# Performance work log

Hardware: AMD Instinct MI355X
Metric: run time of the kernel (lower is better)

The kernel has to match this reference:

```python
import jax, jax.numpy as jnp
import numpy as np

N_NODES = 100000
N_EDGES = 400000
D = 128

def _mlp_ln(x, W1, b1, W2, b2, W3, b3, gamma, beta):
    h = jax.nn.relu(x @ W1 + b1)
    h = jax.nn.relu(h @ W2 + b2)
    h = h @ W3 + b3
    mu = jnp.mean(h, axis=-1, keepdims=True)
    var = jnp.var(h, axis=-1, keepdims=True)
    return (h - mu) * jax.lax.rsqrt(var + 1e-5) * gamma + beta


def setup_inputs() -> dict:
    key = jax.random.key(0)
    ks = jax.random.split(key, 12)
    s = lambda fan_in: 1.0 / np.sqrt(fan_in)
    inp = {
        'node_features': jax.random.normal(ks[0], (1, N_NODES, D), jnp.float32),
        'edge_features': jax.random.normal(ks[1], (1, N_EDGES, D), jnp.float32),
        'senders': jax.random.randint(ks[2], (1, N_EDGES), 0, N_NODES, jnp.int32),
        'receivers': jax.random.randint(ks[3], (1, N_EDGES), 0, N_NODES, jnp.int32),
        'e_W1': jax.random.normal(ks[4], (3 * D, D), jnp.float32) * s(3 * D),
        'e_b1': jnp.zeros((D,), jnp.float32),
        'e_W2': jax.random.normal(ks[5], (D, D), jnp.float32) * s(D),
        'e_b2': jnp.zeros((D,), jnp.float32),
        'e_W3': jax.random.normal(ks[6], (D, D), jnp.float32) * s(D),
        'e_b3': jnp.zeros((D,), jnp.float32),
        'e_gamma': jnp.ones((D,), jnp.float32),
        'e_beta': jnp.zeros((D,), jnp.float32),
        'n_W1': jax.random.normal(ks[7], (2 * D, D), jnp.float32) * s(2 * D),
        'n_b1': jnp.zeros((D,), jnp.float32),
        'n_W2': jax.random.normal(ks[8], (D, D), jnp.float32) * s(D),
        'n_b2': jnp.zeros((D,), jnp.float32),
        'n_W3': jax.random.normal(ks[9], (D, D), jnp.float32) * s(D),
        'n_b3': jnp.zeros((D,), jnp.float32),
        'n_gamma': jnp.ones((D,), jnp.float32),
        'n_beta': jnp.zeros((D,), jnp.float32),
    }
    return inp


def reference(node_features, edge_features, senders, receivers,
              e_W1, e_b1, e_W2, e_b2, e_W3, e_b3, e_gamma, e_beta,
              n_W1, n_b1, n_W2, n_b2, n_W3, n_b3, n_gamma, n_beta):
    # batch dim is 1; indexing matches torch.index_select(dim=1, senders[0])
    snd = senders[0]
    rcv = receivers[0]
    nodes = node_features[0]          # [N, D]
    edges = edge_features[0]          # [E, D]

    # edge update: gather, concat, edge MLP
    edge_in = jnp.concatenate([nodes[snd], nodes[rcv], edges], axis=-1)  # [E, 3D]
    new_edges = _mlp_ln(edge_in, e_W1, e_b1, e_W2, e_b2, e_W3, e_b3, e_gamma, e_beta)

    # node update: segment-sum aggregate to receivers, concat, node MLP
    agg = jax.ops.segment_sum(new_edges, rcv, num_segments=nodes.shape[0])  # [N, D]
    node_in = jnp.concatenate([nodes, agg], axis=-1)                        # [N, 2D]
    new_nodes = _mlp_ln(node_in, n_W1, n_b1, n_W2, n_b2, n_W3, n_b3, n_gamma, n_beta)

    # residuals
    new_nodes = new_nodes + nodes
    new_edges = new_edges + edges
    return new_nodes[None], new_edges[None]
```

## Files before the change

### kernel.cpp

```cpp
#include <hip/hip_runtime.h>
#include <stdint.h>

#define NN 100000
#define NE 400000
#define SCAN_B 391

typedef __attribute__((ext_vector_type(4))) float f32x4;
typedef __attribute__((ext_vector_type(8))) short bf16x8;

__device__ __forceinline__ short f2b(float x){
  union { float f; uint32_t u; } v; v.f = x;
  uint32_t r = v.u + 0x7FFFu + ((v.u >> 16) & 1u);
  return (short)(r >> 16);
}
__device__ __forceinline__ float b2f(short x){
  union { uint32_t u; float f; } v; v.u = ((uint32_t)(unsigned short)x) << 16; return v.f;
}
__device__ __forceinline__ bf16x8 pack_bf8(f32x4 a, f32x4 b){
  bf16x8 r;
  r[0]=f2b(a[0]); r[1]=f2b(a[1]); r[2]=f2b(a[2]); r[3]=f2b(a[3]);
  r[4]=f2b(b[0]); r[5]=f2b(b[1]); r[6]=f2b(b[2]); r[7]=f2b(b[3]);
  return r;
}

__global__ void pack_all(const float* __restrict__ eW1, const float* __restrict__ eW2,
                         const float* __restrict__ eW3, const float* __restrict__ nW1,
                         const float* __restrict__ nW2, const float* __restrict__ nW3,
                         short* __restrict__ dst){
  int o = blockIdx.x*256 + threadIdx.x;
  int seg = o >> 14, rem = o & 16383;
  int kt = rem >> 12, g = (rem >> 10) & 3, n = (rem >> 3) & 127, j = rem & 7;
  int k = kt*32 + g*8 + j;
  const float* src = eW1; int koff = 0;
  switch(seg){
    case 0: src=eW1; koff=0;   break;
    case 1: src=eW1; koff=128; break;
    case 2: src=eW1; koff=256; break;
    case 3: src=eW2; break;
    case 4: src=eW3; break;
    case 5: src=nW1; koff=0;   break;
    case 6: src=nW1; koff=128; break;
    case 7: src=nW2; break;
    case 8: src=nW3; break;
  }
  dst[o] = f2b(src[(size_t)(koff+k)*128 + n]);
}

__global__ void k_count(const int* __restrict__ rcv, int* __restrict__ counts){
  int e = blockIdx.x*256 + threadIdx.x;
  if (e < NE) atomicAdd(&counts[rcv[e]], 1);
}
__global__ void k_psum(const int* __restrict__ counts, int* __restrict__ psums){
  __shared__ int red[256];
  int t = threadIdx.x, i = blockIdx.x*256 + t;
  red[t] = (i < NN) ? counts[i] : 0;
  __syncthreads();
  for (int d=128; d; d>>=1){ if (t<d) red[t] += red[t+d]; __syncthreads(); }
  if (!t) psums[blockIdx.x] = red[0];
}
__global__ __launch_bounds__(512) void k_scanp(const int* __restrict__ psums, int* __restrict__ bbase){
  __shared__ int ps[512];
  int t = threadIdx.x;
  int v = (t < SCAN_B) ? psums[t] : 0;
  ps[t] = v; __syncthreads();
  for (int d=1; d<512; d<<=1){
    int x = (t>=d) ? ps[t-d] : 0;
    __syncthreads();
    ps[t] += x;
    __syncthreads();
  }
  if (t < SCAN_B) bbase[t] = ps[t] - v;
}
__global__ void k_local(const int* __restrict__ counts, const int* __restrict__ bbase,
                        int* __restrict__ offsets, int* __restrict__ cursor){
  __shared__ int ps[256];
  int t = threadIdx.x, i = blockIdx.x*256 + t;
  int v = (i < NN) ? counts[i] : 0;
  ps[t] = v; __syncthreads();
  for (int d=1; d<256; d<<=1){
    int x = (t>=d) ? ps[t-d] : 0;
    __syncthreads();
    ps[t] += x;
    __syncthreads();
  }
  int excl = bbase[blockIdx.x] + ps[t] - v;
  if (i < NN){ offsets[i] = excl; cursor[i] = excl; }
  if (i == 0) offsets[NN] = NE;
}
__global__ void k_scatter(const int* __restrict__ rcv, int* __restrict__ cursor,
                          int* __restrict__ pos){
  int e = blockIdx.x*256 + threadIdx.x;
  if (e < NE) pos[e] = atomicAdd(&cursor[rcv[e]], 1);
}

__global__ __launch_bounds__(512,4) void compute_T(
    const float* __restrict__ nodef, const short* __restrict__ wp,
    short* __restrict__ Tt, int nrows)
{
  __shared__ __align__(16) short Ws[16384];
  const int tid=threadIdx.x, lane=tid&63, wid=tid>>6, l16=lane&15, hi=lane>>4;
  const int row0 = blockIdx.x*128;
  const int arow_l = wid*16 + l16;
  const int arow_c = min(row0 + arow_l, nrows-1);
  const float* s = nodef + (size_t)arow_c*128;

  bf16x8 af[4];
  #pragma unroll
  for (int kt=0; kt<4; kt++){
    int ko = kt*32 + hi*8;
    af[kt] = pack_bf8(*(const f32x4*)(s+ko), *(const f32x4*)(s+ko+4));
  }
  int4 w[4];
  #pragma unroll
  for (int i=0;i<4;i++) w[i] = ((const int4*)wp)[tid + 512*i];

  for (int o=0; o<2; o++){
    if (o) __syncthreads();
    #pragma unroll
    for (int i=0;i<4;i++) ((int4*)Ws)[tid + 512*i] = w[i];
    if (o < 1){
      #pragma unroll
      for (int i=0;i<4;i++) w[i] = ((const int4*)(wp + 16384))[tid + 512*i];
    }
    __syncthreads();
    f32x4 acc[8];
    #pragma unroll
    for (int t=0;t<8;t++) acc[t] = (f32x4)(0.0f);
    #pragma unroll
    for (int kt=0;kt<4;kt++){
      #pragma unroll
      for (int t=0;t<8;t++){
        bf16x8 bw = *(const bf16x8*)&Ws[kt*4096 + hi*1024 + (t*16+l16)*8];
        acc[t] = __builtin_amdgcn_mfma_f32_16x16x32_bf16(af[kt], bw, acc[t], 0,0,0);
      }
    }
    __syncthreads();
    #pragma unroll
    for (int t=0;t<8;t++){
      int col = t*16 + l16;
      #pragma unroll
      for (int r=0;r<4;r++){
        int row = wid*16 + hi*4 + r;
        *(short*)((char*)Ws + row*256 + ((col*2) ^ ((row&7)<<4))) = f2b(acc[t][r]);
      }
    }
    #pragma unroll
    for (int u=0;u<4;u++){
      int q = lane + u*64;
      int r16 = q >> 4, c = q & 15;
      int rl = wid*16 + r16;
      int grow = row0 + rl;
      if (grow < nrows){
        bf16x8 v = *(const bf16x8*)((char*)Ws + rl*256 + ((c*16) ^ ((rl&7)<<4)));
        *(bf16x8*)(Tt + (size_t)grow*256 + o*128 + c*8) = v;
      }
    }
  }
}

#define WSTAGE(NEXT) do{ __syncthreads(); \
  _Pragma("unroll") for(int i=0;i<4;i++) ((int4*)Ws)[tid + 512*i] = w[i]; \
  if ((NEXT) != nullptr){ _Pragma("unroll") for(int i=0;i<4;i++) w[i] = ((const int4*)(NEXT))[tid + 512*i]; } \
  __syncthreads(); }while(0)

#define MM_G() do{ _Pragma("unroll") for(int kt=0;kt<4;kt++){ \
  _Pragma("unroll") for(int t=0;t<8;t++){ \
    bf16x8 bw = *(const bf16x8*)&Ws[kt*4096 + hi*1024 + (t*16+l16)*8]; \
    acc[t] = __builtin_amdgcn_mfma_f32_16x16x32_bf16(afg[kt], bw, acc[t], 0,0,0);} } }while(0)

#define MM_H() do{ _Pragma("unroll") for(int kt=0;kt<4;kt++){ \
  bf16x8 afv = *(const bf16x8*)((char*)HGs + arow_l*256 + ((kt*64 + hi*16) ^ ((arow_l&7)<<4))); \
  _Pragma("unroll") for(int t=0;t<8;t++){ \
    bf16x8 bw = *(const bf16x8*)&Ws[kt*4096 + hi*1024 + (t*16+l16)*8]; \
    acc[t] = __builtin_amdgcn_mfma_f32_16x16x32_bf16(afv, bw, acc[t], 0,0,0);} } }while(0)

#define EPI_RELU(BP, ADDG) do{ \
  _Pragma("unroll") for (int t=0;t<8;t++){ \
    int col=t*16+l16; float bb=(BP)[col]; \
    _Pragma("unroll") for (int r=0;r<4;r++){ \
      int row=wid*16+hi*4+r; \
      float g=0.0f; \
      if (ADDG) g=b2f(*(const short*)((char*)HGs+row*256+((col*2)^((row&7)<<4)))); \
      float v=fmaxf(acc[t][r]+g+bb,0.0f); \
      *(short*)((char*)HGs+row*256+((col*2)^((row&7)<<4)))=f2b(v); \
      acc[t][r]=0.0f; \
    } } }while(0)

template<int MODE>
__global__ __launch_bounds__(512,4) void gnb_mlp(
    const float* __restrict__ nodef, const float* __restrict__ edgef,
    const int* __restrict__ snd, const int* __restrict__ rcv,
    const int* __restrict__ off, const int* __restrict__ pos,
    const short* __restrict__ Tt, short* __restrict__ Ey,
    const short* __restrict__ W1a, const short* __restrict__ W1b,
    const short* __restrict__ W2, const short* __restrict__ W3,
    const float* __restrict__ b1p, const float* __restrict__ b2p, const float* __restrict__ b3p,
    const float* __restrict__ gmp, const float* __restrict__ btp,
    float* __restrict__ outp, int nrows)
{
  __shared__ __align__(16) short Ws[16384];
  __shared__ __align__(16) short HGs[16384];

  const int tid=threadIdx.x, lane=tid&63, wid=tid>>6, l16=lane&15, hi=lane>>4;
  const int row0 = blockIdx.x*128;
  const int arow_l = wid*16 + l16;
  const int arow_c = min(row0 + arow_l, nrows-1);

  int4 w[4];
  #pragma unroll
  for (int i=0;i<4;i++) w[i] = ((const int4*)W1a)[tid + 512*i];

  if (MODE==0){
    bf16x8 ga[4], gb[4];
    #pragma unroll
    for (int u=0;u<4;u++){
      int q = tid + u*512, gr = q >> 4, c = q & 15;
      int grow = row0 + gr;
      int si = snd[grow], ri = rcv[grow];
      ga[u] = *(const bf16x8*)(Tt + (size_t)si*256 + c*8);
      gb[u] = *(const bf16x8*)(Tt + (size_t)ri*256 + 128 + c*8);
    }
    #pragma unroll
    for (int u=0;u<4;u++){
      int q = tid + u*512, gr = q >> 4, c = q & 15;
      bf16x8 o8;
      #pragma unroll
      for (int j=0;j<8;j++) o8[j] = f2b(b2f(ga[u][j]) + b2f(gb[u][j]));
      *(bf16x8*)((char*)HGs + gr*256 + ((c*16) ^ ((gr&7)<<4))) = o8;
    }
  } else {
    #pragma unroll
    for (int u=0;u<4;u++){
      int q = tid + u*512, gr = q >> 4, c = q & 15;
      int grow = row0 + gr;
      float s8[8] = {0,0,0,0,0,0,0,0};
      if (grow < nrows){
        int jb = off[grow], je = off[grow+1];
        for (int j=jb;j<je;j++){
          bf16x8 v = *(const bf16x8*)(Ey + (size_t)j*128 + c*8);
          #pragma unroll
          for (int k=0;k<8;k++) s8[k] += b2f(v[k]);
        }
      }
      bf16x8 o8;
      #pragma unroll
      for (int k=0;k<8;k++) o8[k] = f2b(s8[k]);
      *(bf16x8*)((char*)HGs + gr*256 + ((c*16) ^ ((gr&7)<<4))) = o8;
    }
  }

  WSTAGE((MODE==0) ? W2 : W1b);

  const float* s1 = (MODE==0) ? (edgef + (size_t)arow_c*128) : (nodef + (size_t)arow_c*128);
  bf16x8 afg[4];
  #pragma unroll
  for (int kt=0;kt<4;kt++){
    int ko = kt*32 + hi*8;
    afg[kt] = pack_bf8(*(const f32x4*)(s1+ko), *(const f32x4*)(s1+ko+4));
  }

  f32x4 acc[8];
  #pragma unroll
  for (int t=0;t<8;t++) acc[t] = (f32x4)(0.0f);

  MM_G();
  if (MODE==1){
    WSTAGE(W2);
    MM_H();
  }
  EPI_RELU(b1p, (MODE==0));
  WSTAGE(W3);
  MM_H();
  EPI_RELU(b2p, false);
  WSTAGE((const short*)nullptr);
  MM_H();

  float ps[4] = {0,0,0,0}, pq[4] = {0,0,0,0};
  #pragma unroll
  for (int t=0;t<8;t++){
    float bb = b3p[t*16+l16];
    #pragma unroll
    for (int r=0;r<4;r++){
      float v = acc[t][r] + bb;
      acc[t][r] = v;
      ps[r] += v; pq[r] += v*v;
    }
  }
  #pragma unroll
  for (int m=1;m<16;m<<=1){
    #pragma unroll
    for (int r=0;r<4;r++){
      ps[r] += __shfl_xor(ps[r], m);
      pq[r] += __shfl_xor(pq[r], m);
    }
  }
  float mu[4], rs[4];
  #pragma unroll
  for (int r=0;r<4;r++){
    mu[r] = ps[r] * (1.0f/128.0f);
    float var = pq[r] * (1.0f/128.0f) - mu[r]*mu[r];
    rs[r] = rsqrtf(var + 1e-5f);
  }

  #pragma unroll
  for (int t=0;t<8;t++){
    int col = t*16 + l16;
    float gm = gmp[col], be = btp[col];
    #pragma unroll
    for (int r=0;r<4;r++){
      float y = (acc[t][r]-mu[r])*rs[r]*gm + be;
      int row = wid*16 + hi*4 + r;
      *(short*)((char*)HGs + row*256 + ((col*2) ^ ((row&7)<<4))) = f2b(y);
    }
  }

  #pragma unroll
  for (int u=0;u<4;u++){
    int q = lane + u*64;
    int r16 = q >> 4, c = q & 15;
    int rl = wid*16 + r16;
    int grow = row0 + rl;
    bf16x8 v = *(const bf16x8*)((char*)HGs + rl*256 + ((c*16) ^ ((rl&7)<<4)));
    if (MODE==0){
      const float* ef = edgef + (size_t)grow*128 + c*8;
      f32x4 e0 = *(const f32x4*)ef, e1 = *(const f32x4*)(ef+4);
      f32x4 o0, o1;
      #pragma unroll
      for (int j=0;j<4;j++){ o0[j] = b2f(v[j]) + e0[j]; o1[j] = b2f(v[j+4]) + e1[j]; }
      float* op = outp + (size_t)grow*128 + c*8;
      *(f32x4*)op = o0; *(f32x4*)(op+4) = o1;
      int p = pos[grow];
      *(bf16x8*)(Ey + (size_t)p*128 + c*8) = v;
    } else {
      if (grow < nrows){
        const float* nf = nodef + (size_t)grow*128 + c*8;
        f32x4 e0 = *(const f32x4*)nf, e1 = *(const f32x4*)(nf+4);
        f32x4 o0, o1;
        #pragma unroll
        for (int j=0;j<4;j++){ o0[j] = b2f(v[j]) + e0[j]; o1[j] = b2f(v[j+4]) + e1[j]; }
        float* op = outp + (size_t)grow*128 + c*8;
        *(f32x4*)op = o0; *(f32x4*)(op+4) = o1;
      }
    }
  }
}

extern "C" void kernel_launch(void* const* d_in, const int* in_sizes, int n_in,
                              void* d_out, int out_size, void* d_ws, size_t ws_size,
                              hipStream_t stream)
{
  (void)in_sizes; (void)n_in; (void)out_size; (void)ws_size;
  const float* nodef = (const float*)d_in[0];
  const float* edgef = (const float*)d_in[1];
  const int*   snd   = (const int*)d_in[2];
  const int*   rcv   = (const int*)d_in[3];
  const float* eW1 = (const float*)d_in[4];
  const float* eb1 = (const float*)d_in[5];
  const float* eW2 = (const float*)d_in[6];
  const float* eb2 = (const float*)d_in[7];
  const float* eW3 = (const float*)d_in[8];
  const float* eb3 = (const float*)d_in[9];
  const float* egm = (const float*)d_in[10];
  const float* ebt = (const float*)d_in[11];
  const float* nW1 = (const float*)d_in[12];
  const float* nb1 = (const float*)d_in[13];
  const float* nW2 = (const float*)d_in[14];
  const float* nb2 = (const float*)d_in[15];
  const float* nW3 = (const float*)d_in[16];
  const float* nb3 = (const float*)d_in[17];
  const float* ngm = (const float*)d_in[18];
  const float* nbt = (const float*)d_in[19];

  char* wsb = (char*)d_ws;
  short* Tt = (short*)wsb;
  short* Ey = (short*)(wsb + (size_t)NN*256*2);
  int* counts  = (int*)(wsb + (size_t)NN*256*2 + (size_t)NE*128*2);
  int* offsets = counts + NN;
  int* cursor  = offsets + NN + 8;
  int* psums   = cursor + NN;
  int* bbase   = psums + 512;
  int* pos     = bbase + 512;
  short* wp    = (short*)(pos + NE);

  hipMemsetAsync(counts, 0, (size_t)NN*4, stream);
  k_count<<<(NE+255)/256,256,0,stream>>>(rcv, counts);
  k_psum<<<SCAN_B,256,0,stream>>>(counts, psums);
  k_scanp<<<1,512,0,stream>>>(psums, bbase);
  k_local<<<SCAN_B,256,0,stream>>>(counts, bbase, offsets, cursor);
  k_scatter<<<(NE+255)/256,256,0,stream>>>(rcv, cursor, pos);

  pack_all<<<576,256,0,stream>>>(eW1,eW2,eW3,nW1,nW2,nW3,wp);
  compute_T<<<(NN+127)/128,512,0,stream>>>(nodef, wp, Tt, NN);

  float* out_nodes = (float*)d_out;
  float* out_edges = out_nodes + (size_t)NN*128;

  gnb_mlp<0><<<NE/128,512,0,stream>>>(nodef, edgef, snd, rcv, offsets, pos, Tt, Ey,
      wp+2*16384, (const short*)nullptr, wp+3*16384, wp+4*16384,
      eb1,eb2,eb3, egm,ebt, out_edges, NE);
  gnb_mlp<1><<<(NN+127)/128,512,0,stream>>>(nodef, edgef, snd, rcv, offsets, pos, Tt, Ey,
      wp+5*16384, wp+6*16384, wp+7*16384, wp+8*16384,
      nb1,nb2,nb3, ngm,nbt, out_nodes, NN);
}
```

Before: 440.3 us.

## Read MLP weight fragments directly from global memory instead of LDS staging

```diff
diff --git a/kernel.cpp b/kernel.cpp
--- a/kernel.cpp
+++ b/kernel.cpp
@@ -158,21 +158,16 @@
   }
 }
 
-#define WSTAGE(NEXT) do{ __syncthreads(); \
-  _Pragma("unroll") for(int i=0;i<4;i++) ((int4*)Ws)[tid + 512*i] = w[i]; \
-  if ((NEXT) != nullptr){ _Pragma("unroll") for(int i=0;i<4;i++) w[i] = ((const int4*)(NEXT))[tid + 512*i]; } \
-  __syncthreads(); }while(0)
-
-#define MM_G() do{ _Pragma("unroll") for(int kt=0;kt<4;kt++){ \
-  _Pragma("unroll") for(int t=0;t<8;t++){ \
-    bf16x8 bw = *(const bf16x8*)&Ws[kt*4096 + hi*1024 + (t*16+l16)*8]; \
-    acc[t] = __builtin_amdgcn_mfma_f32_16x16x32_bf16(afg[kt], bw, acc[t], 0,0,0);} } }while(0)
-
-#define MM_H() do{ _Pragma("unroll") for(int kt=0;kt<4;kt++){ \
+#define BW(WP,KT,T) (*(const bf16x8*)&(WP)[(KT)*4096 + hi*1024 + ((T)*16+l16)*8])
+
+#define MM_G(WP) do{ _Pragma("unroll") for(int kt=0;kt<4;kt++){ \
+  _Pragma("unroll") for(int t=0;t<8;t++) \
+    acc[t] = __builtin_amdgcn_mfma_f32_16x16x32_bf16(afg[kt], BW(WP,kt,t), acc[t], 0,0,0); } }while(0)
+
+#define MM_H(WP) do{ _Pragma("unroll") for(int kt=0;kt<4;kt++){ \
   bf16x8 afv = *(const bf16x8*)((char*)HGs + arow_l*256 + ((kt*64 + hi*16) ^ ((arow_l&7)<<4))); \
-  _Pragma("unroll") for(int t=0;t<8;t++){ \
-    bf16x8 bw = *(const bf16x8*)&Ws[kt*4096 + hi*1024 + (t*16+l16)*8]; \
-    acc[t] = __builtin_amdgcn_mfma_f32_16x16x32_bf16(afv, bw, acc[t], 0,0,0);} } }while(0)
+  _Pragma("unroll") for(int t=0;t<8;t++) \
+    acc[t] = __builtin_amdgcn_mfma_f32_16x16x32_bf16(afv, BW(WP,kt,t), acc[t], 0,0,0); } }while(0)
 
 #define EPI_RELU(BP, ADDG) do{ \
   _Pragma("unroll") for (int t=0;t<8;t++){ \
@@ -187,7 +182,7 @@
     } } }while(0)
 
 template<int MODE>
-__global__ __launch_bounds__(512,4) void gnb_mlp(
+__global__ __launch_bounds__(256,5) void gnb_mlp(
     const float* __restrict__ nodef, const float* __restrict__ edgef,
     const int* __restrict__ snd, const int* __restrict__ rcv,
     const int* __restrict__ off, const int* __restrict__ pos,
@@ -198,23 +193,18 @@
     const float* __restrict__ gmp, const float* __restrict__ btp,
     float* __restrict__ outp, int nrows)
 {
-  __shared__ __align__(16) short Ws[16384];
-  __shared__ __align__(16) short HGs[16384];
+  __shared__ __align__(16) short HGs[8192];
 
   const int tid=threadIdx.x, lane=tid&63, wid=tid>>6, l16=lane&15, hi=lane>>4;
-  const int row0 = blockIdx.x*128;
+  const int row0 = blockIdx.x*64;
   const int arow_l = wid*16 + l16;
   const int arow_c = min(row0 + arow_l, nrows-1);
 
-  int4 w[4];
-  #pragma unroll
-  for (int i=0;i<4;i++) w[i] = ((const int4*)W1a)[tid + 512*i];
-
   if (MODE==0){
     bf16x8 ga[4], gb[4];
     #pragma unroll
     for (int u=0;u<4;u++){
-      int q = tid + u*512, gr = q >> 4, c = q & 15;
+      int q = tid + u*256, gr = q >> 4, c = q & 15;
       int grow = row0 + gr;
       int si = snd[grow], ri = rcv[grow];
       ga[u] = *(const bf16x8*)(Tt + (size_t)si*256 + c*8);
@@ -222,7 +212,7 @@
     }
     #pragma unroll
     for (int u=0;u<4;u++){
-      int q = tid + u*512, gr = q >> 4, c = q & 15;
+      int q = tid + u*256, gr = q >> 4, c = q & 15;
       bf16x8 o8;
       #pragma unroll
       for (int j=0;j<8;j++) o8[j] = f2b(b2f(ga[u][j]) + b2f(gb[u][j]));
@@ -231,7 +221,7 @@
   } else {
     #pragma unroll
     for (int u=0;u<4;u++){
-      int q = tid + u*512, gr = q >> 4, c = q & 15;
+      int q = tid + u*256, gr = q >> 4, c = q & 15;
       int grow = row0 + gr;
       float s8[8] = {0,0,0,0,0,0,0,0};
       if (grow < nrows){
@@ -249,8 +239,6 @@
     }
   }
 
-  WSTAGE((MODE==0) ? W2 : W1b);
-
   const float* s1 = (MODE==0) ? (edgef + (size_t)arow_c*128) : (nodef + (size_t)arow_c*128);
   bf16x8 afg[4];
   #pragma unroll
@@ -259,21 +247,18 @@
     afg[kt] = pack_bf8(*(const f32x4*)(s1+ko), *(const f32x4*)(s1+ko+4));
   }
 
+  __syncthreads();
+
   f32x4 acc[8];
   #pragma unroll
   for (int t=0;t<8;t++) acc[t] = (f32x4)(0.0f);
 
-  MM_G();
-  if (MODE==1){
-    WSTAGE(W2);
-    MM_H();
-  }
+  MM_G(W1a);
+  if (MODE==1) MM_H(W1b);
   EPI_RELU(b1p, (MODE==0));
-  WSTAGE(W3);
-  MM_H();
+  MM_H(W2);
   EPI_RELU(b2p, false);
-  WSTAGE((const short*)nullptr);
-  MM_H();
+  MM_H(W3);
 
   float ps[4] = {0,0,0,0}, pq[4] = {0,0,0,0};
   #pragma unroll
@@ -395,10 +380,10 @@
   float* out_nodes = (float*)d_out;
   float* out_edges = out_nodes + (size_t)NN*128;
 
-  gnb_mlp<0><<<NE/128,512,0,stream>>>(nodef, edgef, snd, rcv, offsets, pos, Tt, Ey,
+  gnb_mlp<0><<<NE/64,256,0,stream>>>(nodef, edgef, snd, rcv, offsets, pos, Tt, Ey,
       wp+2*16384, (const short*)nullptr, wp+3*16384, wp+4*16384,
       eb1,eb2,eb3, egm,ebt, out_edges, NE);
-  gnb_mlp<1><<<(NN+127)/128,512,0,stream>>>(nodef, edgef, snd, rcv, offsets, pos, Tt, Ey,
+  gnb_mlp<1><<<(NN+63)/64,256,0,stream>>>(nodef, edgef, snd, rcv, offsets, pos, Tt, Ey,
       wp+5*16384, wp+6*16384, wp+7*16384, wp+8*16384,
       nb1,nb2,nb3, ngm,nbt, out_nodes, NN);
 }
```

After: 571.0 us. +29.7%, slower.

## Add gathered node projections via identity MFMA instead of LDS staging

Applied to the files above, without the earlier changes.

```diff
diff --git a/kernel.cpp b/kernel.cpp
--- a/kernel.cpp
+++ b/kernel.cpp
@@ -174,14 +174,12 @@
     bf16x8 bw = *(const bf16x8*)&Ws[kt*4096 + hi*1024 + (t*16+l16)*8]; \
     acc[t] = __builtin_amdgcn_mfma_f32_16x16x32_bf16(afv, bw, acc[t], 0,0,0);} } }while(0)
 
-#define EPI_RELU(BP, ADDG) do{ \
+#define EPI_RELU(BP) do{ \
   _Pragma("unroll") for (int t=0;t<8;t++){ \
     int col=t*16+l16; float bb=(BP)[col]; \
     _Pragma("unroll") for (int r=0;r<4;r++){ \
       int row=wid*16+hi*4+r; \
-      float g=0.0f; \
-      if (ADDG) g=b2f(*(const short*)((char*)HGs+row*256+((col*2)^((row&7)<<4)))); \
-      float v=fmaxf(acc[t][r]+g+bb,0.0f); \
+      float v=fmaxf(acc[t][r]+bb,0.0f); \
       *(short*)((char*)HGs+row*256+((col*2)^((row&7)<<4)))=f2b(v); \
       acc[t][r]=0.0f; \
     } } }while(0)
@@ -210,23 +208,17 @@
   #pragma unroll
   for (int i=0;i<4;i++) w[i] = ((const int4*)W1a)[tid + 512*i];
 
+  bf16x8 ga[4], gb[4];
   if (MODE==0){
-    bf16x8 ga[4], gb[4];
-    #pragma unroll
-    for (int u=0;u<4;u++){
-      int q = tid + u*512, gr = q >> 4, c = q & 15;
-      int grow = row0 + gr;
-      int si = snd[grow], ri = rcv[grow];
-      ga[u] = *(const bf16x8*)(Tt + (size_t)si*256 + c*8);
-      gb[u] = *(const bf16x8*)(Tt + (size_t)ri*256 + 128 + c*8);
-    }
-    #pragma unroll
-    for (int u=0;u<4;u++){
-      int q = tid + u*512, gr = q >> 4, c = q & 15;
-      bf16x8 o8;
-      #pragma unroll
-      for (int j=0;j<8;j++) o8[j] = f2b(b2f(ga[u][j]) + b2f(gb[u][j]));
-      *(bf16x8*)((char*)HGs + gr*256 + ((c*16) ^ ((gr&7)<<4))) = o8;
+    int si = snd[row0 + arow_l];
+    int ri = rcv[row0 + arow_l];
+    const short* ts = Tt + (size_t)si*256;
+    const short* tr = Tt + (size_t)ri*256 + 128;
+    #pragma unroll
+    for (int kt=0;kt<4;kt++){
+      int ko = kt*32 + hi*8;
+      ga[kt] = *(const bf16x8*)(ts + ko);
+      gb[kt] = *(const bf16x8*)(tr + ko);
     }
   } else {
     #pragma unroll
@@ -264,14 +256,33 @@
   for (int t=0;t<8;t++) acc[t] = (f32x4)(0.0f);
 
   MM_G();
-  if (MODE==1){
+
+  if (MODE==0){
+    bf16x8 bI[2];
+    #pragma unroll
+    for (int s=0;s<2;s++){
+      bf16x8 z;
+      #pragma unroll
+      for (int j=0;j<8;j++) z[j] = 0;
+      if (hi == 2*s + (l16>>3)) z[l16&7] = (short)0x3F80;
+      bI[s] = z;
+    }
+    #pragma unroll
+    for (int kt=0;kt<4;kt++){
+      bf16x8 gf;
+      #pragma unroll
+      for (int j=0;j<8;j++) gf[j] = f2b(b2f(ga[kt][j]) + b2f(gb[kt][j]));
+      acc[2*kt+0] = __builtin_amdgcn_mfma_f32_16x16x32_bf16(gf, bI[0], acc[2*kt+0], 0,0,0);
+      acc[2*kt+1] = __builtin_amdgcn_mfma_f32_16x16x32_bf16(gf, bI[1], acc[2*kt+1], 0,0,0);
+    }
+  } else {
     WSTAGE(W2);
     MM_H();
   }
-  EPI_RELU(b1p, (MODE==0));
+  EPI_RELU(b1p);
   WSTAGE(W3);
   MM_H();
-  EPI_RELU(b2p, false);
+  EPI_RELU(b2p);
   WSTAGE((const short*)nullptr);
   MM_H();
 
```

After: 446.3 us. About the same (+1.4%).
